# Performance work log

Measured on AMD Instinct MI355X. Metric: run time of the kernel, lower is better.

The kernel has to match this reference:

```python
import jax, jax.numpy as jnp
import numpy as np

NUM_EXPERTS = 8
TOP_K = 2
HIDDEN = 1024
INTER_TOTAL = 8192  # intermediate_size * experts_per_rank
B, S = 2, 2048


def setup_inputs() -> dict:
    key = jax.random.key(0)
    k1, k2, k3, k4, k5, k6 = jax.random.split(key, 6)
    T = B * S
    x = jax.random.normal(k1, (B, S, HIDDEN), dtype=jnp.float32)
    scores = jax.random.uniform(k2, (T, NUM_EXPERTS), dtype=jnp.float32)
    expert_weights = jax.random.uniform(k3, (T, TOP_K), dtype=jnp.float32)
    top_experts = jax.random.randint(k4, (T, TOP_K), 0, NUM_EXPERTS, dtype=jnp.int32)
    w1 = jax.random.normal(k5, (HIDDEN, INTER_TOTAL), dtype=jnp.float32) * 0.02
    w2 = jax.random.normal(k6, (INTER_TOTAL, HIDDEN), dtype=jnp.float32) * 0.02
    return {"x": x, "scores": scores, "expert_weights": expert_weights,
            "top_experts": top_experts, "w1": w1, "w2": w2}


def reference(x, scores, expert_weights, top_experts, w1, w2):
    # forward_once with expert_parallel_size == 1 (dropless MoE dispatch/combine).
    in_shape = x.shape
    T = in_shape[0] * in_shape[1]
    H = in_shape[-1]
    x_flat = x.reshape(T, H)

    flat_experts = top_experts.reshape(-1)          # [T*top_k]
    flat_weights = expert_weights.reshape(-1)       # [T*top_k]

    # ops.sort: stable radix sort of routed copies by expert id
    order = jnp.argsort(flat_experts, stable=True)  # "indices"
    token_idx = order // TOP_K                      # source token per sorted slot

    # padded_gather: bucket tokens per expert (padding rows are zeros and
    # pass through the bias-free MLP as zeros, so they never affect output)
    xg = x_flat[token_idx]                          # [T*top_k, H]

    # MLP: w1 -> gelu(tanh approx) -> w2
    h = jax.nn.gelu(xg @ w1, approximate=True)      # [T*top_k, inter*E]
    y = h @ w2                                      # [T*top_k, H]

    # padded_scatter: weighted combine back to token order
    w_sorted = flat_weights[order]
    out = jnp.zeros((T, H), dtype=x.dtype).at[token_idx].add(w_sorted[:, None] * y)
    return out.reshape(in_shape)
```

## Files before the change

### kernel.cpp

```cpp
#include <hip/hip_runtime.h>
#include <hip/hip_bf16.h>
#include <math.h>

#define HID 1024
#define INTER 8192
#define TT 4096

typedef __bf16 bf16x8 __attribute__((ext_vector_type(8)));
typedef float f32x4 __attribute__((ext_vector_type(4)));

__device__ __forceinline__ void gll16(const void* g, void* l) {
    __builtin_amdgcn_global_load_lds(
        (const __attribute__((address_space(1))) void*)g,
        (__attribute__((address_space(3))) void*)l, 16, 0, 0);
}

__device__ __forceinline__ bf16x8 ds_read128(unsigned addr) {
    bf16x8 r;
    asm volatile("ds_read_b128 %0, %1" : "=v"(r) : "v"(addr));
    return r;
}

__global__ void k_prep(const float* __restrict__ x, const float* __restrict__ ew,
                       __hip_bfloat16* __restrict__ xb, float* __restrict__ s,
                       int n4, int T) {
    int stride = gridDim.x * blockDim.x;
    for (int i = blockIdx.x * blockDim.x + threadIdx.x; i < n4; i += stride) {
        float4 v = ((const float4*)x)[i];
        __hip_bfloat16* o = xb + (size_t)i * 4;
        o[0] = __float2bfloat16(v.x);
        o[1] = __float2bfloat16(v.y);
        o[2] = __float2bfloat16(v.z);
        o[3] = __float2bfloat16(v.w);
    }
    for (int t = blockIdx.x * blockDim.x + threadIdx.x; t < T; t += stride)
        s[t] = ew[2 * t] + ew[2 * t + 1];
}

__global__ void k_tcast(const float* __restrict__ in, __hip_bfloat16* __restrict__ out,
                        int R, int C) {
    __shared__ float tile[32][33];
    const int tx = threadIdx.x & 31, ty = threadIdx.x >> 5;
    const int br = blockIdx.y * 32, bc = blockIdx.x * 32;
#pragma unroll
    for (int j = 0; j < 32; j += 8)
        tile[ty + j][tx] = in[(size_t)(br + ty + j) * C + bc + tx];
    __syncthreads();
#pragma unroll
    for (int j = 0; j < 32; j += 8)
        out[(size_t)(bc + ty + j) * R + br + tx] = __float2bfloat16(tile[tx][ty + j]);
}

template <int EPI>
__global__ __launch_bounds__(512, 2) void k_gemm8(
    const __hip_bfloat16* __restrict__ A, const __hip_bfloat16* __restrict__ Bt,
    __hip_bfloat16* __restrict__ hOut, float* __restrict__ fOut,
    const float* __restrict__ s, int Kfull, int nt, int Nout) {
    __shared__ __hip_bfloat16 sA[2][2][128][64];
    __shared__ __hip_bfloat16 sB[2][2][128][64];
    const int tid = threadIdx.x;
    const int lane = tid & 63, wid = tid >> 6;
    const int wr = wid >> 2, wc = wid & 3;

    const int nwg = gridDim.x * gridDim.y;
    const int wg = blockIdx.y * gridDim.x + blockIdx.x;
    const int swz = (wg & 7) * (nwg >> 3) + (wg >> 3);
    const int brow = (swz / gridDim.x) * 256;
    const int bcol = (swz % gridDim.x) * 256;
    const size_t kbase = (size_t)blockIdx.z * ((size_t)nt * 64);

    const int rstage = tid >> 3;
    const int colsw = (((tid & 7) ^ (rstage & 7)) << 3);
    const __hip_bfloat16* gA = A + (size_t)(brow + rstage) * Kfull + kbase + colsw;
    const __hip_bfloat16* gB = Bt + (size_t)(bcol + rstage) * Kfull + kbase + colsw;
    const size_t rowStep = (size_t)64 * Kfull;
    const size_t halfStep = (size_t)128 * Kfull;

    char* ldsA0 = (char*)&sA[0][0][0][0] + wid * 1024;
    char* ldsB0 = (char*)&sB[0][0][0][0] + wid * 1024;

    const unsigned baseA = (unsigned)(uintptr_t)&sA[0][0][0][0];
    const unsigned baseB = (unsigned)(uintptr_t)&sB[0][0][0][0];
    const unsigned g0 = (((lane >> 4)) ^ (lane & 7)) << 4;
    const unsigned g1 = ((4 + (lane >> 4)) ^ (lane & 7)) << 4;
    const unsigned rdA0 = baseA + wr * 16384 + (lane & 15) * 128 + g0;
    const unsigned rdA1 = baseA + wr * 16384 + (lane & 15) * 128 + g1;
    const unsigned rdB0 = baseB + (wc >> 1) * 16384 + (wc & 1) * 8192 + (lane & 15) * 128 + g0;
    const unsigned rdB1 = baseB + (wc >> 1) * 16384 + (wc & 1) * 8192 + (lane & 15) * 128 + g1;

    f32x4 acc[8][4] = {};
    bf16x8 aF[4][2], b01[2][2], b23[2][2];

#define STAGE_A(buf, half, t)                                              \
    do {                                                                   \
        const __hip_bfloat16* _g = gA + (half) * halfStep + (size_t)(t) * 64; \
        char* _l = ldsA0 + (buf) * 32768 + (half) * 16384;                 \
        gll16(_g, _l);                                                     \
        gll16(_g + rowStep, _l + 8192);                                    \
    } while (0)
#define STAGE_B(buf, half, t)                                              \
    do {                                                                   \
        const __hip_bfloat16* _g = gB + (half) * halfStep + (size_t)(t) * 64; \
        char* _l = ldsB0 + (buf) * 32768 + (half) * 16384;                 \
        gll16(_g, _l);                                                     \
        gll16(_g + rowStep, _l + 8192);                                    \
    } while (0)
#define PIN() __builtin_amdgcn_sched_barrier(0)
#define BAR()                              \
    do {                                   \
        PIN();                             \
        __builtin_amdgcn_s_barrier();      \
        PIN();                             \
    } while (0)
#define WAIT_LGKM0() __builtin_amdgcn_s_waitcnt(0xC07F)
#define WAIT_LGKM8() __builtin_amdgcn_s_waitcnt(0xC87F)
#define WAIT_VM4() __builtin_amdgcn_s_waitcnt(0x0F74)
#define WAIT_VM0() __builtin_amdgcn_s_waitcnt(0x0F70)
#define RDA(buf, r, ks) ds_read128(((ks) ? rdA1 : rdA0) + (buf) * 32768u + (r) * 2048u)
#define RDB(buf, r, ks) ds_read128(((ks) ? rdB1 : rdB0) + (buf) * 32768u + (r) * 2048u)
#define MM_Q(mbase, nbase, bfr)                                                   \
    _Pragma("unroll") for (int ks = 0; ks < 2; ++ks)                              \
    _Pragma("unroll") for (int m = 0; m < 4; ++m)                                 \
    _Pragma("unroll") for (int n = 0; n < 2; ++n)                                 \
        acc[(mbase) + m][(nbase) + n] = __builtin_amdgcn_mfma_f32_16x16x32_bf16(  \
            aF[m][ks], bfr[n][ks], acc[(mbase) + m][(nbase) + n], 0, 0, 0);
#define MFMA_PHASE(mbase, nbase, bfr)     \
    do {                                  \
        WAIT_LGKM0();                     \
        PIN();                            \
        __builtin_amdgcn_s_setprio(1);    \
        MM_Q(mbase, nbase, bfr);          \
        __builtin_amdgcn_s_setprio(0);    \
        PIN();                            \
    } while (0)

    STAGE_B(0, 0, 0);
    STAGE_B(0, 1, 0);
    STAGE_A(0, 0, 0);
    STAGE_A(0, 1, 0);
    STAGE_B(1, 0, 1);
    STAGE_B(1, 1, 1);
    WAIT_VM4();
    BAR();

    const int iters = nt >> 1;
    for (int i = 0; i < iters; ++i) {
        const bool full = (i + 1 < iters);
        const int t1 = 2 * i + 1, t2 = 2 * i + 2, t3 = 2 * i + 3;

#pragma unroll
        for (int m = 0; m < 4; ++m) {
            aF[m][0] = RDA(0, m, 0);
            aF[m][1] = RDA(0, m, 1);
        }
#pragma unroll
        for (int n = 0; n < 2; ++n) {
            b01[n][0] = RDB(0, n, 0);
            b01[n][1] = RDB(0, n, 1);
        }
        STAGE_A(1, 0, t1);
        WAIT_LGKM8();
        BAR();
        MFMA_PHASE(0, 0, b01);
        BAR();

#pragma unroll
        for (int n = 0; n < 2; ++n) {
            b23[n][0] = RDB(0, 2 + n, 0);
            b23[n][1] = RDB(0, 2 + n, 1);
        }
        STAGE_A(1, 1, t1);
        BAR();
        MFMA_PHASE(0, 2, b23);
        BAR();

#pragma unroll
        for (int m = 0; m < 4; ++m) {
            aF[m][0] = RDA(0, 4 + m, 0);
            aF[m][1] = RDA(0, 4 + m, 1);
        }
        if (full) STAGE_B(0, 0, t2);
        BAR();
        MFMA_PHASE(4, 2, b23);
        BAR();

        if (full) STAGE_B(0, 1, t2);
        BAR();
        MFMA_PHASE(4, 0, b01);
        if (full)
            WAIT_VM4();
        else
            WAIT_VM0();
        BAR();

#pragma unroll
        for (int m = 0; m < 4; ++m) {
            aF[m][0] = RDA(1, m, 0);
            aF[m][1] = RDA(1, m, 1);
        }
#pragma unroll
        for (int n = 0; n < 2; ++n) {
            b01[n][0] = RDB(1, n, 0);
            b01[n][1] = RDB(1, n, 1);
        }
        if (full) STAGE_A(0, 0, t2);
        WAIT_LGKM8();
        BAR();
        MFMA_PHASE(0, 0, b01);
        BAR();

#pragma unroll
        for (int n = 0; n < 2; ++n) {
            b23[n][0] = RDB(1, 2 + n, 0);
            b23[n][1] = RDB(1, 2 + n, 1);
        }
        if (full) STAGE_A(0, 1, t2);
        BAR();
        MFMA_PHASE(0, 2, b23);
        BAR();

#pragma unroll
        for (int m = 0; m < 4; ++m) {
            aF[m][0] = RDA(1, 4 + m, 0);
            aF[m][1] = RDA(1, 4 + m, 1);
        }
        if (full) STAGE_B(1, 0, t3);
        BAR();
        MFMA_PHASE(4, 2, b23);
        BAR();

        if (full) STAGE_B(1, 1, t3);
        BAR();
        MFMA_PHASE(4, 0, b01);
        if (full)
            WAIT_VM4();
        else
            WAIT_VM0();
        BAR();
    }

    const int orow = brow + wr * 128 + ((lane >> 4) << 2);
    const int ocol = bcol + wc * 64 + (lane & 15);
#pragma unroll
    for (int m = 0; m < 8; ++m) {
#pragma unroll
        for (int j = 0; j < 4; ++j) {
            const int r = orow + m * 16 + j;
            const size_t ro = (size_t)r * Nout;
            if (EPI == 0) {
#pragma unroll
                for (int n = 0; n < 4; ++n) {
                    float v = acc[m][n][j];
                    float u = 1.5957691216057308f * (v + 0.044715f * v * v * v);
                    float g = v / (1.0f + __expf(-u));
                    hOut[ro + ocol + n * 16] = __float2bfloat16(g);
                }
            } else {
                const float sc = s[r];
#pragma unroll
                for (int n = 0; n < 4; ++n)
                    unsafeAtomicAdd(&fOut[ro + ocol + n * 16], sc * acc[m][n][j]);
            }
        }
    }
#undef STAGE_A
#undef STAGE_B
#undef PIN
#undef BAR
#undef WAIT_LGKM0
#undef WAIT_LGKM8
#undef WAIT_VM4
#undef WAIT_VM0
#undef RDA
#undef RDB
#undef MM_Q
#undef MFMA_PHASE
}

extern "C" void kernel_launch(void* const* d_in, const int* in_sizes, int n_in,
                              void* d_out, int out_size, void* d_ws, size_t ws_size,
                              hipStream_t stream) {
    const float* x = (const float*)d_in[0];
    const float* ew = (const float*)d_in[2];
    const float* w1 = (const float*)d_in[4];
    const float* w2 = (const float*)d_in[5];
    float* out = (float*)d_out;

    char* ws = (char*)d_ws;
    float* s = (float*)ws;
    __hip_bfloat16* xb = (__hip_bfloat16*)(ws + 16384);
    __hip_bfloat16* w1t = (__hip_bfloat16*)(ws + 16384 + 8388608);
    __hip_bfloat16* w2t = (__hip_bfloat16*)(ws + 16384 + 8388608 + 16777216);
    __hip_bfloat16* h = (__hip_bfloat16*)(ws + 16384 + 8388608 + 2 * 16777216);

    k_prep<<<1024, 256, 0, stream>>>(x, ew, xb, s, (TT * HID) / 4, TT);

    dim3 t1(INTER / 32, HID / 32);
    k_tcast<<<t1, 256, 0, stream>>>(w1, w1t, HID, INTER);
    dim3 t2(HID / 32, INTER / 32);
    k_tcast<<<t2, 256, 0, stream>>>(w2, w2t, INTER, HID);

    dim3 g1(INTER / 256, TT / 256, 1);
    k_gemm8<0><<<g1, 512, 0, stream>>>(xb, w1t, h, nullptr, nullptr, HID, HID / 64, INTER);

    hipMemsetAsync(out, 0, (size_t)TT * HID * sizeof(float), stream);
    dim3 g2(HID / 256, TT / 256, 4);
    k_gemm8<1><<<g2, 512, 0, stream>>>(h, w2t, nullptr, out, s, INTER, 2048 / 64, HID);
}
```

Before: 210.9 us.

## Restructure GEMM global-to-LDS staging so each wave loads its own fragment rows

Each wave now stages the A and B rows that its own MFMA reads consume, in four contiguous 8-row chunks, instead of the earlier interleaved half-tile layout. The prefetch schedule changes from staggered half-tile loads with a partial vmcnt wait to loading the whole next tile during the first two phases and waiting for all loads at the end of each half-iteration. This aims to simplify address generation and improve locality of LDS writes. The trade-off is a shallower prefetch: B is no longer loaded two tiles ahead, and the full vmcnt(0) wait may expose global memory latency.

```diff
diff --git a/kernel.cpp b/kernel.cpp
--- a/kernel.cpp
+++ b/kernel.cpp
@@ -69,15 +69,17 @@
     const int bcol = (swz % gridDim.x) * 256;
     const size_t kbase = (size_t)blockIdx.z * ((size_t)nt * 64);
 
-    const int rstage = tid >> 3;
-    const int colsw = (((tid & 7) ^ (rstage & 7)) << 3);
-    const __hip_bfloat16* gA = A + (size_t)(brow + rstage) * Kfull + kbase + colsw;
-    const __hip_bfloat16* gB = Bt + (size_t)(bcol + rstage) * Kfull + kbase + colsw;
-    const size_t rowStep = (size_t)64 * Kfull;
-    const size_t halfStep = (size_t)128 * Kfull;
-
-    char* ldsA0 = (char*)&sA[0][0][0][0] + wid * 1024;
-    char* ldsB0 = (char*)&sB[0][0][0][0] + wid * 1024;
+    const int colsw = (((lane & 7) ^ (lane >> 3)) << 3);
+    const int qA0 = (wid & 3) * 4;
+    const int bh = (wid >> 1) & 1;
+    const int qB0 = ((wid & 1) | ((wid >> 2) << 1)) * 4;
+    const __hip_bfloat16* gA2 =
+        A + (size_t)(brow + wr * 128 + qA0 * 8 + (lane >> 3)) * Kfull + kbase + colsw;
+    const __hip_bfloat16* gB2 =
+        Bt + (size_t)(bcol + bh * 128 + qB0 * 8 + (lane >> 3)) * Kfull + kbase + colsw;
+    char* ldsA2 = (char*)&sA[0][0][0][0] + wr * 16384 + qA0 * 1024;
+    char* ldsB2 = (char*)&sB[0][0][0][0] + bh * 16384 + qB0 * 1024;
+    const size_t chunkStep = (size_t)8 * Kfull;
 
     const unsigned baseA = (unsigned)(uintptr_t)&sA[0][0][0][0];
     const unsigned baseB = (unsigned)(uintptr_t)&sB[0][0][0][0];
@@ -91,19 +93,17 @@
     f32x4 acc[8][4] = {};
     bf16x8 aF[4][2], b01[2][2], b23[2][2];
 
-#define STAGE_A(buf, half, t)                                              \
-    do {                                                                   \
-        const __hip_bfloat16* _g = gA + (half) * halfStep + (size_t)(t) * 64; \
-        char* _l = ldsA0 + (buf) * 32768 + (half) * 16384;                 \
-        gll16(_g, _l);                                                     \
-        gll16(_g + rowStep, _l + 8192);                                    \
-    } while (0)
-#define STAGE_B(buf, half, t)                                              \
-    do {                                                                   \
-        const __hip_bfloat16* _g = gB + (half) * halfStep + (size_t)(t) * 64; \
-        char* _l = ldsB0 + (buf) * 32768 + (half) * 16384;                 \
-        gll16(_g, _l);                                                     \
-        gll16(_g + rowStep, _l + 8192);                                    \
+#define STAGE_A2(buf, t)                                                       \
+    do {                                                                       \
+        _Pragma("unroll") for (int j = 0; j < 4; ++j)                          \
+            gll16(gA2 + (size_t)j * chunkStep + (size_t)(t) * 64,              \
+                  ldsA2 + (buf) * 32768 + j * 1024);                           \
+    } while (0)
+#define STAGE_B2(buf, t)                                                       \
+    do {                                                                       \
+        _Pragma("unroll") for (int j = 0; j < 4; ++j)                          \
+            gll16(gB2 + (size_t)j * chunkStep + (size_t)(t) * 64,              \
+                  ldsB2 + (buf) * 32768 + j * 1024);                           \
     } while (0)
 #define PIN() __builtin_amdgcn_sched_barrier(0)
 #define BAR()                              \
@@ -114,7 +114,6 @@
     } while (0)
 #define WAIT_LGKM0() __builtin_amdgcn_s_waitcnt(0xC07F)
 #define WAIT_LGKM8() __builtin_amdgcn_s_waitcnt(0xC87F)
-#define WAIT_VM4() __builtin_amdgcn_s_waitcnt(0x0F74)
 #define WAIT_VM0() __builtin_amdgcn_s_waitcnt(0x0F70)
 #define RDA(buf, r, ks) ds_read128(((ks) ? rdA1 : rdA0) + (buf) * 32768u + (r) * 2048u)
 #define RDB(buf, r, ks) ds_read128(((ks) ? rdB1 : rdB0) + (buf) * 32768u + (r) * 2048u)
@@ -134,19 +133,15 @@
         PIN();                            \
     } while (0)
 
-    STAGE_B(0, 0, 0);
-    STAGE_B(0, 1, 0);
-    STAGE_A(0, 0, 0);
-    STAGE_A(0, 1, 0);
-    STAGE_B(1, 0, 1);
-    STAGE_B(1, 1, 1);
-    WAIT_VM4();
+    STAGE_A2(0, 0);
+    STAGE_B2(0, 0);
+    WAIT_VM0();
     BAR();
 
     const int iters = nt >> 1;
     for (int i = 0; i < iters; ++i) {
         const bool full = (i + 1 < iters);
-        const int t1 = 2 * i + 1, t2 = 2 * i + 2, t3 = 2 * i + 3;
+        const int t1 = 2 * i + 1, t2 = 2 * i + 2;
 
 #pragma unroll
         for (int m = 0; m < 4; ++m) {
@@ -158,7 +153,7 @@
             b01[n][0] = RDB(0, n, 0);
             b01[n][1] = RDB(0, n, 1);
         }
-        STAGE_A(1, 0, t1);
+        STAGE_A2(1, t1);
         WAIT_LGKM8();
         BAR();
         MFMA_PHASE(0, 0, b01);
@@ -169,7 +164,7 @@
             b23[n][0] = RDB(0, 2 + n, 0);
             b23[n][1] = RDB(0, 2 + n, 1);
         }
-        STAGE_A(1, 1, t1);
+        STAGE_B2(1, t1);
         BAR();
         MFMA_PHASE(0, 2, b23);
         BAR();
@@ -179,18 +174,13 @@
             aF[m][0] = RDA(0, 4 + m, 0);
             aF[m][1] = RDA(0, 4 + m, 1);
         }
-        if (full) STAGE_B(0, 0, t2);
         BAR();
         MFMA_PHASE(4, 2, b23);
         BAR();
 
-        if (full) STAGE_B(0, 1, t2);
         BAR();
         MFMA_PHASE(4, 0, b01);
-        if (full)
-            WAIT_VM4();
-        else
-            WAIT_VM0();
+        WAIT_VM0();
         BAR();
 
 #pragma unroll
@@ -203,7 +193,7 @@
             b01[n][0] = RDB(1, n, 0);
             b01[n][1] = RDB(1, n, 1);
         }
-        if (full) STAGE_A(0, 0, t2);
+        if (full) STAGE_A2(0, t2);
         WAIT_LGKM8();
         BAR();
         MFMA_PHASE(0, 0, b01);
@@ -214,7 +204,7 @@
             b23[n][0] = RDB(1, 2 + n, 0);
             b23[n][1] = RDB(1, 2 + n, 1);
         }
-        if (full) STAGE_A(0, 1, t2);
+        if (full) STAGE_B2(0, t2);
         BAR();
         MFMA_PHASE(0, 2, b23);
         BAR();
@@ -224,18 +214,13 @@
             aF[m][0] = RDA(1, 4 + m, 0);
             aF[m][1] = RDA(1, 4 + m, 1);
         }
-        if (full) STAGE_B(1, 0, t3);
         BAR();
         MFMA_PHASE(4, 2, b23);
         BAR();
 
-        if (full) STAGE_B(1, 1, t3);
         BAR();
         MFMA_PHASE(4, 0, b01);
-        if (full)
-            WAIT_VM4();
-        else
-            WAIT_VM0();
+        WAIT_VM0();
         BAR();
     }
 
@@ -263,13 +248,12 @@
             }
         }
     }
-#undef STAGE_A
-#undef STAGE_B
+#undef STAGE_A2
+#undef STAGE_B2
 #undef PIN
 #undef BAR
 #undef WAIT_LGKM0
 #undef WAIT_LGKM8
-#undef WAIT_VM4
 #undef WAIT_VM0
 #undef RDA
 #undef RDB
```

Measured after the change: 211.3 us. Within noise of the previous version (+0.2%).
